# Kernel optimization log

Hardware: AMD Instinct MI355X
Metric: run time of the kernel (lower is better)

## Reference

```python
import jax, jax.numpy as jnp
import numpy as np

NUM_NODES = 100000
NUM_REL = 8
HIDDEN = 128
NUM_EDGES = 1600000
NUM_LAYERS = 2


def setup_inputs() -> dict:
    key = jax.random.key(0)
    k1, k2, k3, k4, k5 = jax.random.split(key, 5)
    x = jnp.arange(NUM_NODES, dtype=jnp.int64)
    edge_index = jax.random.randint(k1, (2, NUM_EDGES), 0, NUM_NODES, dtype=jnp.int64)
    edge_type = jax.random.randint(k2, (NUM_EDGES,), 0, NUM_REL, dtype=jnp.int64)
    emb = jax.random.normal(k3, (NUM_NODES, HIDDEN), dtype=jnp.float32) * 0.1
    W = jax.random.normal(k4, (NUM_LAYERS, NUM_REL, HIDDEN, HIDDEN), dtype=jnp.float32) * (1.0 / np.sqrt(HIDDEN))
    root = jax.random.normal(k5, (NUM_LAYERS, HIDDEN, HIDDEN), dtype=jnp.float32) * (1.0 / np.sqrt(HIDDEN))
    bias = jnp.zeros((NUM_LAYERS, HIDDEN), dtype=jnp.float32)
    return {"x": x, "edge_index": edge_index, "edge_type": edge_type,
            "emb": emb, "W": W, "root": root, "bias": bias}


def _rgcn_conv(h, src, dst, etype, W_l, root_l, bias_l):
    # h: [N, d]; W_l: [R, d, d]
    n = h.shape[0]
    r = W_l.shape[0]
    # Transform all nodes by every relation weight: [R, N, d]
    xW = jnp.einsum('nd,rdf->rnf', h, W_l)
    # Per-edge message gathered by (relation, source): [E, d]
    msg = xW[etype, src]
    # Mean-normalize per (target node, relation), matching PyG aggr='mean'
    seg = dst * r + etype  # combined (node, relation) segment id
    cnt = jax.ops.segment_sum(jnp.ones(msg.shape[0], dtype=h.dtype), seg,
                              num_segments=n * r)
    norm = 1.0 / jnp.maximum(cnt[seg], 1.0)
    agg = jax.ops.segment_sum(msg * norm[:, None], dst, num_segments=n)
    return agg + h @ root_l + bias_l


def reference(x, edge_index, edge_type, emb, W, root, bias):
    src, dst = edge_index[0], edge_index[1]
    h = emb[x]  # embedding lookup
    for l in range(NUM_LAYERS):
        h = _rgcn_conv(h, src, dst, edge_type, W[l], root[l], bias[l])
        h = jax.nn.relu(h)
    return h
```

## Files before the change

kernel.cpp:

```cpp
#include <hip/hip_runtime.h>

typedef unsigned int u32;
typedef unsigned short u16;
typedef __attribute__((ext_vector_type(8))) short short8;
typedef __attribute__((ext_vector_type(4))) float f32x4;

#define DD 128
#define RREL 8
#define KCAT 1152
#define SCAN_CHUNK 4096

static __device__ __forceinline__ u16 f2bf(float f) {
  u32 u = __builtin_bit_cast(u32, f);
  u32 r = (u + 0x7fffu + ((u >> 16) & 1u)) >> 16;
  return (u16)r;
}
static __device__ __forceinline__ float bflo(u32 v) { return __builtin_bit_cast(float, v << 16); }
static __device__ __forceinline__ float bfhi(u32 v) { return __builtin_bit_cast(float, v & 0xffff0000u); }

__global__ __launch_bounds__(256) void k_convw(const float* __restrict__ W,
                                               const float* __restrict__ root,
                                               u16* __restrict__ wt) {
  int t = blockIdx.x * 256 + threadIdx.x;
  if (t >= 2 * DD * KCAT) return;
  int l = t / (DD * KCAT);
  int rem = t - l * DD * KCAT;
  int col = rem / KCAT;
  int k = rem - col * KCAT;
  float v;
  if (k < DD) {
    v = root[(size_t)l * DD * DD + k * DD + col];
  } else {
    int r = (k - DD) >> 7, kk = (k - DD) & 127;
    v = W[(size_t)(l * RREL + r) * DD * DD + kk * DD + col];
  }
  wt[(size_t)l * DD * KCAT + col * KCAT + k] = f2bf(v);
}

__global__ __launch_bounds__(256) void k_gather(const int* __restrict__ x,
                                                const float* __restrict__ emb,
                                                u16* __restrict__ acat, int N) {
  int t = blockIdx.x * 256 + threadIdx.x;
  if (t >= N * 16) return;
  int node = t >> 4, part = t & 15;
  const float4* e4 = (const float4*)(emb + (size_t)x[node] * DD + part * 8);
  float4 f0 = e4[0], f1 = e4[1];
  uint4 u;
  u.x = (u32)f2bf(f0.x) | ((u32)f2bf(f0.y) << 16);
  u.y = (u32)f2bf(f0.z) | ((u32)f2bf(f0.w) << 16);
  u.z = (u32)f2bf(f1.x) | ((u32)f2bf(f1.y) << 16);
  u.w = (u32)f2bf(f1.z) | ((u32)f2bf(f1.w) << 16);
  *(uint4*)(acat + (size_t)node * KCAT + part * 8) = u;
}

__global__ __launch_bounds__(256) void k_hist(const int* __restrict__ ei,
                                              const int* __restrict__ et,
                                              int* __restrict__ cnt, int E) {
  int e = blockIdx.x * 256 + threadIdx.x;
  if (e >= E) return;
  int dst = ei[E + e];
  atomicAdd(&cnt[dst * 8 + et[e]], 1);
}

__global__ __launch_bounds__(256) void k_scan_reduce(const int* __restrict__ cnt,
                                                     int* __restrict__ blksum, int nseg) {
  __shared__ int s[256];
  int b = blockIdx.x, t = threadIdx.x;
  int base = b * SCAN_CHUNK;
  int sum = 0;
  for (int i = 0; i < 16; ++i) {
    int idx = base + i * 256 + t;
    if (idx < nseg) sum += cnt[idx];
  }
  s[t] = sum;
  __syncthreads();
  for (int st = 128; st > 0; st >>= 1) {
    if (t < st) s[t] += s[t + st];
    __syncthreads();
  }
  if (t == 0) blksum[b] = s[0];
}

__global__ void k_scan_top(int* __restrict__ blksum, int nblk, int* __restrict__ off,
                           int nseg, int E) {
  if (threadIdx.x == 0 && blockIdx.x == 0) {
    int run = 0;
    for (int b = 0; b < nblk; ++b) { int v = blksum[b]; blksum[b] = run; run += v; }
    off[nseg] = E;
  }
}

__global__ __launch_bounds__(256) void k_scan_write(const int* __restrict__ cnt,
                                                    const int* __restrict__ blksum,
                                                    int* __restrict__ off, int nseg) {
  __shared__ int s[256];
  int b = blockIdx.x, t = threadIdx.x;
  int base = b * SCAN_CHUNK + t * 16;
  int v[16];
  int sum = 0;
#pragma unroll
  for (int i = 0; i < 16; ++i) {
    int idx = base + i;
    v[i] = (idx < nseg) ? cnt[idx] : 0;
    sum += v[i];
  }
  s[t] = sum;
  __syncthreads();
  for (int st = 1; st < 256; st <<= 1) {
    int add = (t >= st) ? s[t - st] : 0;
    __syncthreads();
    s[t] += add;
    __syncthreads();
  }
  int run = blksum[b] + s[t] - sum;
#pragma unroll
  for (int i = 0; i < 16; ++i) {
    int idx = base + i;
    if (idx < nseg) off[idx] = run;
    run += v[i];
  }
}

__global__ __launch_bounds__(256) void k_scatter(const int* __restrict__ ei,
                                                 const int* __restrict__ et,
                                                 const int* __restrict__ off,
                                                 int* __restrict__ fill,
                                                 int* __restrict__ sorted, int E) {
  int e = blockIdx.x * 256 + threadIdx.x;
  if (e >= E) return;
  int src = ei[e], dst = ei[E + e];
  int seg = dst * 8 + et[e];
  int pos = off[seg] + atomicAdd(&fill[seg], 1);
  sorted[pos] = src;
}

__global__ __launch_bounds__(256) void k_agg(const int* __restrict__ off,
                                             const int* __restrict__ sorted,
                                             u16* acat, int nseg) {
  int wave = threadIdx.x >> 6, lane = threadIdx.x & 63;
  int sub = lane >> 4, quad = lane & 15;
  int seg = blockIdx.x * 16 + wave * 4 + sub;
  if (seg >= nseg) return;
  int s = off[seg], e = off[seg + 1];
  float a0 = 0.f, a1 = 0.f, a2 = 0.f, a3 = 0.f, a4 = 0.f, a5 = 0.f, a6 = 0.f, a7 = 0.f;
  for (int j = s; j < e; ++j) {
    int src = sorted[j];
    uint4 v = *(const uint4*)(acat + (size_t)src * KCAT + quad * 8);
    a0 += bflo(v.x); a1 += bfhi(v.x);
    a2 += bflo(v.y); a3 += bfhi(v.y);
    a4 += bflo(v.z); a5 += bfhi(v.z);
    a6 += bflo(v.w); a7 += bfhi(v.w);
  }
  float norm = (e > s) ? 1.0f / (float)(e - s) : 0.f;
  uint4 w;
  w.x = (u32)f2bf(a0 * norm) | ((u32)f2bf(a1 * norm) << 16);
  w.y = (u32)f2bf(a2 * norm) | ((u32)f2bf(a3 * norm) << 16);
  w.z = (u32)f2bf(a4 * norm) | ((u32)f2bf(a5 * norm) << 16);
  w.w = (u32)f2bf(a6 * norm) | ((u32)f2bf(a7 * norm) << 16);
  int dst = seg >> 3, r = seg & 7;
  *(uint4*)(acat + (size_t)dst * KCAT + DD + r * DD + quad * 8) = w;
}

template <bool LAST>
__global__ __launch_bounds__(256) void k_gemm(u16* acat, const u16* __restrict__ wt,
                                              const float* __restrict__ bias,
                                              float* __restrict__ dout, int M) {
  __shared__ uint4 ldsB[2048];
  int tid = threadIdx.x, wave = tid >> 6, lane = tid & 63;
  int rowbase = blockIdx.x * 64 + wave * 16;
  int arow = rowbase + (lane & 15);
  int arc = arow < M ? arow : M - 1;
  int klane = (lane >> 4) << 3;
  f32x4 acc[8];
#pragma unroll
  for (int c = 0; c < 8; ++c) acc[c] = (f32x4)0.f;
  for (int kt = 0; kt < 9; ++kt) {
    __syncthreads();
#pragma unroll
    for (int i = 0; i < 8; ++i) {
      int cid = i * 256 + tid;
      int col = cid >> 4, cb = cid & 15;
      uint4 v = *(const uint4*)(wt + (size_t)col * KCAT + kt * DD + cb * 8);
      ldsB[col * 16 + (cb ^ (col & 7))] = v;
    }
    __syncthreads();
#pragma unroll
    for (int kc = 0; kc < 4; ++kc) {
      short8 a = *(const short8*)(acat + (size_t)arc * KCAT + kt * DD + kc * 32 + klane);
      int chunk = kc * 4 + (lane >> 4);
#pragma unroll
      for (int c = 0; c < 8; ++c) {
        int col = c * 16 + (lane & 15);
        const short8* bp = (const short8*)&ldsB[col * 16 + (chunk ^ (col & 7))];
        acc[c] = __builtin_amdgcn_mfma_f32_16x16x32_bf16(a, *bp, acc[c], 0, 0, 0);
      }
    }
  }
  int crow0 = rowbase + ((lane >> 4) << 2);
  int ccol = lane & 15;
#pragma unroll
  for (int c = 0; c < 8; ++c) {
    int col = c * 16 + ccol;
    float bv = bias[col];
#pragma unroll
    for (int i = 0; i < 4; ++i) {
      int row = crow0 + i;
      if (row < M) {
        float v = fmaxf(acc[c][i] + bv, 0.f);
        if (LAST) dout[(size_t)row * DD + col] = v;
        else acat[(size_t)row * KCAT + col] = f2bf(v);
      }
    }
  }
}

extern "C" void kernel_launch(void* const* d_in, const int* in_sizes, int n_in,
                              void* d_out, int out_size, void* d_ws, size_t ws_size,
                              hipStream_t stream) {
  const int* x = (const int*)d_in[0];
  const int* ei = (const int*)d_in[1];
  const int* et = (const int*)d_in[2];
  const float* emb = (const float*)d_in[3];
  const float* W = (const float*)d_in[4];
  const float* root = (const float*)d_in[5];
  const float* bias = (const float*)d_in[6];

  const int N = in_sizes[0];
  const int E = in_sizes[2];
  const int NSEG = N * RREL;

  size_t o = 0;
  auto al = [&](size_t b) { size_t r = o; o = (o + b + 255) & ~(size_t)255; return r; };
  size_t off_o = al(((size_t)NSEG + 1) * 4);
  size_t cnt_o = al((size_t)NSEG * 4);
  size_t fill_o = al((size_t)NSEG * 4);
  size_t sorted_o = al((size_t)E * 4);
  size_t blk_o = al(4096);
  size_t wt_o = al((size_t)2 * DD * KCAT * 2);
  size_t acat_o = al((size_t)N * KCAT * 2);
  (void)acat_o;

  char* ws = (char*)d_ws;
  int* off = (int*)(ws + off_o);
  int* cnt = (int*)(ws + cnt_o);
  int* fill = (int*)(ws + fill_o);
  int* sorted = (int*)(ws + sorted_o);
  int* blks = (int*)(ws + blk_o);
  u16* wt = (u16*)(ws + wt_o);
  u16* acat = (u16*)(ws + acat_o);
  float* outf = (float*)d_out;

  k_convw<<<(2 * DD * KCAT + 255) / 256, 256, 0, stream>>>(W, root, wt);
  k_gather<<<(N * 16 + 255) / 256, 256, 0, stream>>>(x, emb, acat, N);
  hipMemsetAsync(cnt, 0, (size_t)NSEG * 4, stream);
  hipMemsetAsync(fill, 0, (size_t)NSEG * 4, stream);
  k_hist<<<(E + 255) / 256, 256, 0, stream>>>(ei, et, cnt, E);
  int nblk = (NSEG + SCAN_CHUNK - 1) / SCAN_CHUNK;
  k_scan_reduce<<<nblk, 256, 0, stream>>>(cnt, blks, NSEG);
  k_scan_top<<<1, 64, 0, stream>>>(blks, nblk, off, NSEG, E);
  k_scan_write<<<nblk, 256, 0, stream>>>(cnt, blks, off, NSEG);
  k_scatter<<<(E + 255) / 256, 256, 0, stream>>>(ei, et, off, fill, sorted, E);

  int gx = (N + 63) / 64;
  k_agg<<<(NSEG + 15) / 16, 256, 0, stream>>>(off, sorted, acat, NSEG);
  k_gemm<false><<<gx, 256, 0, stream>>>(acat, wt, bias, nullptr, N);
  k_agg<<<(NSEG + 15) / 16, 256, 0, stream>>>(off, sorted, acat, NSEG);
  k_gemm<true><<<gx, 256, 0, stream>>>(acat, wt + (size_t)DD * KCAT, bias + DD, outf, N);
}
```

Baseline: 603.0 us.

## Pre-swizzle weight tiles, double-buffer GEMM B loads via direct-to-LDS, widen aggregation

The weight conversion kernel now writes bf16 weights already in the swizzled per-k-tile LDS layout. The GEMM can then copy them with global_load_lds straight into a double-buffered shared tile, prefetching the next k-tile while the current one feeds the MFMAs, and uses 512-thread blocks covering 128 rows. The aggregation kernel gives each lane 16 features instead of 8, packs 8 segments per wave and unrolls the edge loop by two for more memory-level parallelism. The costs are double the LDS per block, a single barrier per k-step, and higher register use in the aggregation kernel.

```diff
diff --git a/kernel.cpp b/kernel.cpp
--- a/kernel.cpp
+++ b/kernel.cpp
@@ -8,6 +8,7 @@
 #define DD 128
 #define RREL 8
 #define KCAT 1152
+#define NKT 9
 #define SCAN_CHUNK 4096
 
 static __device__ __forceinline__ u16 f2bf(float f) {
@@ -20,21 +21,31 @@
 
 __global__ __launch_bounds__(256) void k_convw(const float* __restrict__ W,
                                                const float* __restrict__ root,
-                                               u16* __restrict__ wt) {
+                                               uint4* __restrict__ wt) {
   int t = blockIdx.x * 256 + threadIdx.x;
-  if (t >= 2 * DD * KCAT) return;
-  int l = t / (DD * KCAT);
-  int rem = t - l * DD * KCAT;
-  int col = rem / KCAT;
-  int k = rem - col * KCAT;
-  float v;
-  if (k < DD) {
-    v = root[(size_t)l * DD * DD + k * DD + col];
-  } else {
-    int r = (k - DD) >> 7, kk = (k - DD) & 127;
-    v = W[(size_t)(l * RREL + r) * DD * DD + kk * DD + col];
-  }
-  wt[(size_t)l * DD * KCAT + col * KCAT + k] = f2bf(v);
+  if (t >= 2 * NKT * 2048) return;
+  int l = t / (NKT * 2048);
+  int rem = t - l * (NKT * 2048);
+  int kt = rem >> 11;
+  int pos = rem & 2047;
+  int col = pos >> 4;
+  int cbx = pos & 15;
+  int cb = cbx ^ (col & 7);
+  int k0 = kt * DD + cb * 8;
+  u16 vals[8];
+#pragma unroll
+  for (int i = 0; i < 8; ++i) {
+    int k = k0 + i;
+    float v;
+    if (k < DD) {
+      v = root[(size_t)l * DD * DD + k * DD + col];
+    } else {
+      int km = k - DD;
+      v = W[((size_t)l * RREL + (km >> 7)) * DD * DD + (size_t)(km & 127) * DD + col];
+    }
+    vals[i] = f2bf(v);
+  }
+  wt[t] = *(uint4*)vals;
 }
 
 __global__ __launch_bounds__(256) void k_gather(const int* __restrict__ x,
@@ -134,56 +145,85 @@
   sorted[pos] = src;
 }
 
+static __device__ __forceinline__ void add8(float* a, uint4 v) {
+  a[0] += bflo(v.x); a[1] += bfhi(v.x);
+  a[2] += bflo(v.y); a[3] += bfhi(v.y);
+  a[4] += bflo(v.z); a[5] += bfhi(v.z);
+  a[6] += bflo(v.w); a[7] += bfhi(v.w);
+}
+
 __global__ __launch_bounds__(256) void k_agg(const int* __restrict__ off,
                                              const int* __restrict__ sorted,
                                              u16* acat, int nseg) {
   int wave = threadIdx.x >> 6, lane = threadIdx.x & 63;
-  int sub = lane >> 4, quad = lane & 15;
-  int seg = blockIdx.x * 16 + wave * 4 + sub;
+  int sub = lane >> 3, oct = lane & 7;
+  int seg = blockIdx.x * 32 + wave * 8 + sub;
   if (seg >= nseg) return;
   int s = off[seg], e = off[seg + 1];
-  float a0 = 0.f, a1 = 0.f, a2 = 0.f, a3 = 0.f, a4 = 0.f, a5 = 0.f, a6 = 0.f, a7 = 0.f;
-  for (int j = s; j < e; ++j) {
-    int src = sorted[j];
-    uint4 v = *(const uint4*)(acat + (size_t)src * KCAT + quad * 8);
-    a0 += bflo(v.x); a1 += bfhi(v.x);
-    a2 += bflo(v.y); a3 += bfhi(v.y);
-    a4 += bflo(v.z); a5 += bfhi(v.z);
-    a6 += bflo(v.w); a7 += bfhi(v.w);
+  float a[16];
+#pragma unroll
+  for (int i = 0; i < 16; ++i) a[i] = 0.f;
+  int j = s;
+  for (; j + 2 <= e; j += 2) {
+    int s0 = sorted[j], s1 = sorted[j + 1];
+    const uint4* p0 = (const uint4*)(acat + (size_t)s0 * KCAT + oct * 16);
+    const uint4* p1 = (const uint4*)(acat + (size_t)s1 * KCAT + oct * 16);
+    uint4 v0 = p0[0], v0b = p0[1];
+    uint4 v1 = p1[0], v1b = p1[1];
+    add8(a, v0); add8(a + 8, v0b);
+    add8(a, v1); add8(a + 8, v1b);
+  }
+  if (j < e) {
+    const uint4* p0 = (const uint4*)(acat + (size_t)sorted[j] * KCAT + oct * 16);
+    uint4 v0 = p0[0], v0b = p0[1];
+    add8(a, v0); add8(a + 8, v0b);
   }
   float norm = (e > s) ? 1.0f / (float)(e - s) : 0.f;
-  uint4 w;
-  w.x = (u32)f2bf(a0 * norm) | ((u32)f2bf(a1 * norm) << 16);
-  w.y = (u32)f2bf(a2 * norm) | ((u32)f2bf(a3 * norm) << 16);
-  w.z = (u32)f2bf(a4 * norm) | ((u32)f2bf(a5 * norm) << 16);
-  w.w = (u32)f2bf(a6 * norm) | ((u32)f2bf(a7 * norm) << 16);
+  uint4 w0, w1;
+  w0.x = (u32)f2bf(a[0] * norm) | ((u32)f2bf(a[1] * norm) << 16);
+  w0.y = (u32)f2bf(a[2] * norm) | ((u32)f2bf(a[3] * norm) << 16);
+  w0.z = (u32)f2bf(a[4] * norm) | ((u32)f2bf(a[5] * norm) << 16);
+  w0.w = (u32)f2bf(a[6] * norm) | ((u32)f2bf(a[7] * norm) << 16);
+  w1.x = (u32)f2bf(a[8] * norm) | ((u32)f2bf(a[9] * norm) << 16);
+  w1.y = (u32)f2bf(a[10] * norm) | ((u32)f2bf(a[11] * norm) << 16);
+  w1.z = (u32)f2bf(a[12] * norm) | ((u32)f2bf(a[13] * norm) << 16);
+  w1.w = (u32)f2bf(a[14] * norm) | ((u32)f2bf(a[15] * norm) << 16);
   int dst = seg >> 3, r = seg & 7;
-  *(uint4*)(acat + (size_t)dst * KCAT + DD + r * DD + quad * 8) = w;
+  uint4* outp = (uint4*)(acat + (size_t)dst * KCAT + DD + r * DD + oct * 16);
+  outp[0] = w0;
+  outp[1] = w1;
 }
 
 template <bool LAST>
-__global__ __launch_bounds__(256) void k_gemm(u16* acat, const u16* __restrict__ wt,
+__global__ __launch_bounds__(512) void k_gemm(u16* acat, const uint4* __restrict__ wt,
                                               const float* __restrict__ bias,
                                               float* __restrict__ dout, int M) {
-  __shared__ uint4 ldsB[2048];
+  __shared__ uint4 ldsB[2][2048];
   int tid = threadIdx.x, wave = tid >> 6, lane = tid & 63;
-  int rowbase = blockIdx.x * 64 + wave * 16;
+  int rowbase = blockIdx.x * 128 + wave * 16;
   int arow = rowbase + (lane & 15);
   int arc = arow < M ? arow : M - 1;
   int klane = (lane >> 4) << 3;
   f32x4 acc[8];
 #pragma unroll
   for (int c = 0; c < 8; ++c) acc[c] = (f32x4)0.f;
-  for (int kt = 0; kt < 9; ++kt) {
+
+#define STAGE(KT, BUF)                                                                   \
+  do {                                                                                   \
+    const uint4* gsrc = wt + (size_t)(KT) * 2048;                                        \
+    _Pragma("unroll") for (int i_ = 0; i_ < 4; ++i_) {                                   \
+      int cid_ = i_ * 512 + tid;                                                         \
+      __builtin_amdgcn_global_load_lds(                                                  \
+          (const __attribute__((address_space(1))) uint4*)(gsrc + cid_),                 \
+          (__attribute__((address_space(3))) uint4*)&ldsB[BUF][cid_], 16, 0, 0);         \
+    }                                                                                    \
+  } while (0)
+
+  STAGE(0, 0);
+  for (int kt = 0; kt < NKT; ++kt) {
+    int cur = kt & 1;
     __syncthreads();
-#pragma unroll
-    for (int i = 0; i < 8; ++i) {
-      int cid = i * 256 + tid;
-      int col = cid >> 4, cb = cid & 15;
-      uint4 v = *(const uint4*)(wt + (size_t)col * KCAT + kt * DD + cb * 8);
-      ldsB[col * 16 + (cb ^ (col & 7))] = v;
-    }
-    __syncthreads();
+    if (kt + 1 < NKT) STAGE(kt + 1, cur ^ 1);
 #pragma unroll
     for (int kc = 0; kc < 4; ++kc) {
       short8 a = *(const short8*)(acat + (size_t)arc * KCAT + kt * DD + kc * 32 + klane);
@@ -191,11 +231,13 @@
 #pragma unroll
       for (int c = 0; c < 8; ++c) {
         int col = c * 16 + (lane & 15);
-        const short8* bp = (const short8*)&ldsB[col * 16 + (chunk ^ (col & 7))];
+        const short8* bp = (const short8*)&ldsB[cur][col * 16 + (chunk ^ (col & 7))];
         acc[c] = __builtin_amdgcn_mfma_f32_16x16x32_bf16(a, *bp, acc[c], 0, 0, 0);
       }
     }
   }
+#undef STAGE
+
   int crow0 = rowbase + ((lane >> 4) << 2);
   int ccol = lane & 15;
 #pragma unroll
@@ -236,7 +278,7 @@
   size_t fill_o = al((size_t)NSEG * 4);
   size_t sorted_o = al((size_t)E * 4);
   size_t blk_o = al(4096);
-  size_t wt_o = al((size_t)2 * DD * KCAT * 2);
+  size_t wt_o = al((size_t)2 * NKT * 2048 * 16);
   size_t acat_o = al((size_t)N * KCAT * 2);
   (void)acat_o;
 
@@ -246,11 +288,11 @@
   int* fill = (int*)(ws + fill_o);
   int* sorted = (int*)(ws + sorted_o);
   int* blks = (int*)(ws + blk_o);
-  u16* wt = (u16*)(ws + wt_o);
+  uint4* wt = (uint4*)(ws + wt_o);
   u16* acat = (u16*)(ws + acat_o);
   float* outf = (float*)d_out;
 
-  k_convw<<<(2 * DD * KCAT + 255) / 256, 256, 0, stream>>>(W, root, wt);
+  k_convw<<<(2 * NKT * 2048 + 255) / 256, 256, 0, stream>>>(W, root, wt);
   k_gather<<<(N * 16 + 255) / 256, 256, 0, stream>>>(x, emb, acat, N);
   hipMemsetAsync(cnt, 0, (size_t)NSEG * 4, stream);
   hipMemsetAsync(fill, 0, (size_t)NSEG * 4, stream);
@@ -261,9 +303,9 @@
   k_scan_write<<<nblk, 256, 0, stream>>>(cnt, blks, off, NSEG);
   k_scatter<<<(E + 255) / 256, 256, 0, stream>>>(ei, et, off, fill, sorted, E);
 
-  int gx = (N + 63) / 64;
-  k_agg<<<(NSEG + 15) / 16, 256, 0, stream>>>(off, sorted, acat, NSEG);
-  k_gemm<false><<<gx, 256, 0, stream>>>(acat, wt, bias, nullptr, N);
-  k_agg<<<(NSEG + 15) / 16, 256, 0, stream>>>(off, sorted, acat, NSEG);
-  k_gemm<true><<<gx, 256, 0, stream>>>(acat, wt + (size_t)DD * KCAT, bias + DD, outf, N);
-}
+  int gx = (N + 127) / 128;
+  k_agg<<<(NSEG + 31) / 32, 256, 0, stream>>>(off, sorted, acat, NSEG);
+  k_gemm<false><<<gx, 512, 0, stream>>>(acat, wt, bias, nullptr, N);
+  k_agg<<<(NSEG + 31) / 32, 256, 0, stream>>>(off, sorted, acat, NSEG);
+  k_gemm<true><<<gx, 512, 0, stream>>>(acat, wt + (size_t)NKT * 2048, bias + DD, outf, N);
+}
```

Result: faster. 512.5 us (-15.0%).
